# Kernel tuning notes

Hardware: AMD Instinct MI355X
Metric: run time of the kernel (lower is better)

## Reference

```python
import jax, jax.numpy as jnp
import numpy as np

NUM_CAT = 16
SEG_LENS = np.array([4, 2, 2, 4, 4, 3, 3, 2, 4, 6, 2, 6, 3, 3, 3, 3], dtype=np.int64)
SHIFTS = np.concatenate([[0], np.cumsum(SEG_LENS)[:-1]]).astype(np.int64)
MAX_SEG_COUNT = int(SEG_LENS.max())           # 6
MAX_SEG = int(SHIFTS[-1] + SEG_LENS[-1] - 1)  # 53
IN = 128
N = 65536
EPS = 1e-5  # BatchNorm1d default eps
SLOPE = 0.2  # LeakyReLU negative slope


def setup_inputs() -> dict:
    key = jax.random.key(0)
    ks = jax.random.split(key, 4)
    features = jax.random.normal(ks[0], (N, IN), dtype=jnp.float32)
    category_labels = jax.random.randint(ks[1], (N,), 0, NUM_CAT, dtype=jnp.int64)
    # channel raising MLP: Linear(IN -> NUM_CAT*IN, bias=False)
    W1 = jax.random.normal(ks[2], (IN, NUM_CAT * IN), dtype=jnp.float32) * (1.0 / np.sqrt(IN))
    gamma = jnp.ones((NUM_CAT * IN,), dtype=jnp.float32)
    beta = jnp.zeros((NUM_CAT * IN,), dtype=jnp.float32)
    # UnaryConv weight: xavier_normal over (NUM_CAT, IN, MAX_SEG_COUNT)
    W2 = jax.random.normal(ks[3], (NUM_CAT, IN, MAX_SEG_COUNT), dtype=jnp.float32) * np.sqrt(2.0 / (IN + MAX_SEG_COUNT))
    bias = jnp.zeros((MAX_SEG_COUNT,), dtype=jnp.float32)
    return dict(features=features, W1=W1, gamma=gamma, beta=beta, W2=W2, bias=bias,
                category_labels=category_labels)


def reference(features, W1, gamma, beta, W2, bias, category_labels):
    n = features.shape[0]
    # channel raising: Linear -> BatchNorm1d (batch stats) -> LeakyReLU(0.2)
    h = features @ W1                                   # [N, C*D]
    mean = h.mean(axis=0)
    var = h.var(axis=0)                                 # biased, as in torch BN
    h = (h - mean) / jnp.sqrt(var + EPS) * gamma + beta
    h = jnp.where(h >= 0, h, SLOPE * h)
    # per-category batched matmul classifier
    h = h.reshape(n, NUM_CAT, IN).transpose(1, 0, 2)    # [C, N, D]
    logits_all = jnp.einsum('cnd,cds->cns', h, W2) + bias  # [C, N, S]
    n_idx = jnp.arange(n)
    logits = logits_all[category_labels, n_idx]         # gather: [N, S]
    logsm = jax.nn.log_softmax(logits, axis=-1)
    # scatter into per-category segment ranges of the [N, MAX_SEG+1] output
    shifts = jnp.asarray(SHIFTS)[category_labels]       # [N]
    seg_len = jnp.asarray(SEG_LENS)[category_labels]    # [N]
    s_idx = jnp.arange(MAX_SEG_COUNT)
    valid = s_idx[None, :] < seg_len[:, None]           # [N, S]
    cols = jnp.clip(shifts[:, None] + s_idx[None, :], 0, MAX_SEG)
    vals = jnp.where(valid, logsm, 0.0)                 # invalid slots add 0
    out = jnp.zeros((n, MAX_SEG + 1), dtype=logsm.dtype)
    out = out.at[n_idx[:, None], cols].add(vals)
    return out
```

## Files before the change

### kernel.cpp

```cpp
#include <hip/hip_runtime.h>
#include <hip/hip_bf16.h>

#define NCAT 16

typedef __attribute__((ext_vector_type(8))) short short8v;
typedef __attribute__((ext_vector_type(4))) float float4v;
typedef __attribute__((ext_vector_type(16))) float f32x16;

__constant__ int c_shift[NCAT] = {0,4,6,8,12,16,19,22,24,28,34,36,42,45,48,51};
__constant__ int c_len[NCAT]   = {4,2,2,4,4,3,3,2,4,6,2,6,3,3,3,3};


static inline __device__ unsigned pk2(float lo, float hi) {
  float2 f2; f2.x = lo; f2.y = hi;
  __hip_bfloat162 h = __float22bfloat162_rn(f2);
  unsigned u; __builtin_memcpy(&u, &h, 4);
  return u;
}
static inline __device__ float bf2f(unsigned short v) {
  unsigned u = (unsigned)v << 16;
  float f; __builtin_memcpy(&f, &u, 4);
  return f;
}

template<bool PART>
__global__ __launch_bounds__(1024) void k_stats_m(
    const float* __restrict__ F, const float* __restrict__ W1,
    float* __restrict__ Gdst, unsigned* __restrict__ Gp16,
    float* __restrict__ sv, float* __restrict__ svpart,
    unsigned short* __restrict__ Wlb)
{
  const int tid = threadIdx.x;
  if (blockIdx.x >= 256) {
    const int cat = (int)blockIdx.x - 256;
    for (int e = tid; e < 2048; e += 1024) {
      const int fid = e >> 6, l = e & 63;
      const int ks = fid >> 3, ct = fid & 7;
      const int kb = 32 * ks + 8 * (l >> 4);
      const int c = cat * 128 + 16 * ct + (l & 15);
      uint4 pk;
      pk.x = pk2(W1[(size_t)(kb + 0) * 2048 + c], W1[(size_t)(kb + 1) * 2048 + c]);
      pk.y = pk2(W1[(size_t)(kb + 2) * 2048 + c], W1[(size_t)(kb + 3) * 2048 + c]);
      pk.z = pk2(W1[(size_t)(kb + 4) * 2048 + c], W1[(size_t)(kb + 5) * 2048 + c]);
      pk.w = pk2(W1[(size_t)(kb + 6) * 2048 + c], W1[(size_t)(kb + 7) * 2048 + c]);
      *(uint4*)(Wlb + ((size_t)(cat * 32 + fid) * 64 + l) * 8) = pk;
    }
    return;
  }

  const int rowbase = blockIdx.x * 256;
  const int wid = tid >> 6, lane = tid & 63;
  const int wi = wid >> 2, wj = wid & 3;
  const int i0 = wi * 32, j0 = wj * 32;
  const int lr = lane & 31, lh = lane >> 5;

  f32x16 acc;
  #pragma unroll
  for (int e = 0; e < 16; ++e) acc[e] = 0.f;
  float svacc = 0.f;

  for (int ch = 0; ch < 8; ++ch) {
    #pragma unroll
    for (int h = 0; h < 2; ++h) {
      const int rbase = rowbase + ch * 32 + 16 * h + 8 * lh;
      float fa[8], fb[8];
      #pragma unroll
      for (int j = 0; j < 8; ++j) {
        const float* rp = F + (size_t)(rbase + j) * 128;
        fa[j] = rp[i0 + lr];
        fb[j] = rp[j0 + lr];
      }
      if (wj == 0) {
        #pragma unroll
        for (int j = 0; j < 8; ++j) svacc += fa[j];
      }
      uint4 av4, bv4;
      av4.x = pk2(fa[0], fa[1]); av4.y = pk2(fa[2], fa[3]);
      av4.z = pk2(fa[4], fa[5]); av4.w = pk2(fa[6], fa[7]);
      bv4.x = pk2(fb[0], fb[1]); bv4.y = pk2(fb[2], fb[3]);
      bv4.z = pk2(fb[4], fb[5]); bv4.w = pk2(fb[6], fb[7]);
      acc = __builtin_amdgcn_mfma_f32_32x32x16_bf16(
          __builtin_bit_cast(short8v, av4), __builtin_bit_cast(short8v, bv4),
          acc, 0, 0, 0);
    }
  }

  if (wj == 0) {
    svacc += __shfl_xor(svacc, 32);
    if (lane < 32) {
      if (PART) svpart[blockIdx.x * 128 + i0 + lr] = svacc;
      else      atomicAdd(&sv[i0 + lr], svacc);
    }
  }

  if (PART) {
    unsigned* gp = Gp16 + (size_t)blockIdx.x * 8192;
    #pragma unroll
    for (int t = 0; t < 8; ++t) {
      const int rowe = ((2 * t) & 3) + 8 * (t >> 1) + 4 * lh;
      gp[((i0 + rowe) >> 1) * 128 + j0 + lr] = pk2(acc[2 * t], acc[2 * t + 1]);
    }
  } else {
    #pragma unroll
    for (int reg = 0; reg < 16; ++reg) {
      const int row = (reg & 3) + 8 * (reg >> 2) + 4 * lh;
      atomicAdd(&Gdst[(i0 + row) * 128 + j0 + lr], acc[reg]);
    }
  }
}

__global__ __launch_bounds__(256) void k_reduce(
    const unsigned* __restrict__ Gp16, const float* __restrict__ svpart,
    float* __restrict__ G, float* __restrict__ sv)
{
  const int b = blockIdx.x, tid = threadIdx.x;
  if (b < 64) {
    const int e = b * 128 + (tid >> 1);
    const int half = tid & 1;
    float lo = 0.f, hi = 0.f;
    #pragma unroll 4
    for (int p = half * 128; p < half * 128 + 128; ++p) {
      const unsigned u = Gp16[(size_t)p * 8192 + e];
      lo += bf2f((unsigned short)(u & 0xffffu));
      hi += bf2f((unsigned short)(u >> 16));
    }
    lo += __shfl_xor(lo, 1);
    hi += __shfl_xor(hi, 1);
    if (half == 0) {
      const int pr = e >> 7, col = e & 127;
      G[(2 * pr) * 128 + col]     = lo;
      G[(2 * pr + 1) * 128 + col] = hi;
    }
  } else {
    if (tid < 128) {
      float s = 0.f;
      #pragma unroll 8
      for (int p = 0; p < 256; ++p) s += svpart[p * 128 + tid];
      sv[tid] = s;
    }
  }
}

__global__ __launch_bounds__(256) void k_params(
    const float* __restrict__ G, const float* __restrict__ sv,
    const float* __restrict__ W1, const float* __restrict__ gamma,
    const float* __restrict__ beta, float* __restrict__ scale,
    float* __restrict__ shiftv)
{
  __shared__ float Gl[128][133];
  __shared__ float Wl[128][16];
  __shared__ float redq[16][16];
  __shared__ float redm[16][16];
  const int tid = threadIdx.x;
  const int jb = blockIdx.x * 16;
  for (int i = tid; i < 16384; i += 256) Gl[i >> 7][i & 127] = G[i];
  for (int i = tid; i < 2048; i += 256) {
    int k = i >> 4, col = i & 15;
    Wl[k][col] = W1[(size_t)k * 2048 + jb + col];
  }
  __syncthreads();
  const int col = tid & 15, part = tid >> 4;
  float msq = 0.f, mean = 0.f;
  for (int ii = 0; ii < 8; ++ii) {
    const int i = part * 8 + ii;
    const float wi = Wl[i][col];
    float inner = 0.f;
    #pragma unroll 8
    for (int k = 0; k < 128; ++k) inner = fmaf(Gl[i][k], Wl[k][col], inner);
    msq = fmaf(wi, inner, msq);
  }
  #pragma unroll
  for (int kk = 0; kk < 8; ++kk) {
    const int k = part * 8 + kk;
    mean = fmaf(sv[k], Wl[k][col], mean);
  }
  redq[part][col] = msq;
  redm[part][col] = mean;
  __syncthreads();
  if (tid < 16) {
    float q = 0.f, m = 0.f;
    #pragma unroll
    for (int p = 0; p < 16; ++p) { q += redq[p][tid]; m += redm[p][tid]; }
    m *= (1.f / 65536.f);
    q *= (1.f / 65536.f);
    float var = q - m * m;
    float sc = gamma[jb + tid] * rsqrtf(var + 1e-5f);
    scale[jb + tid] = sc;
    shiftv[jb + tid] = beta[jb + tid] - m * sc;
  }
}

__global__ __launch_bounds__(512, 4) void k_main(
    const float* __restrict__ F, const unsigned short* __restrict__ Wlb,
    const float* __restrict__ W2, const float* __restrict__ bias,
    const float* __restrict__ scale, const float* __restrict__ shiftv,
    const int* __restrict__ lab, float* __restrict__ out)
{
  __shared__ float W2l[16 * 784];
  __shared__ float obuf[128 * 54];
  __shared__ unsigned short lrows[128];
  __shared__ int wcs[2][NCAT];
  __shared__ int loff[NCAT + 1];
  __shared__ unsigned char gcat[32], gsub[32];
  __shared__ int gtot;

  const int tid = threadIdx.x;
  const int blk = (int)blockIdx.x;
  const int wid = tid >> 6, lane = tid & 63;
  const int lrow = lane & 15, lhi = lane >> 4;

  for (int i = tid; i < 12288; i += 512) {
    const int cat = i / 768;
    const int r = i - cat * 768;
    const int c = r / 6, s = r - c * 6;
    W2l[cat * 784 + c * 6 + s + (c >> 3)] = W2[i];
  }
  for (int i = tid; i < 6912; i += 512) obuf[i] = 0.f;

  int myc = 0, myrank = 0;
  if (tid < 128) {
    myc = lab[blk * 128 + tid];
    const unsigned long long lanebit = 1ull << lane;
    #pragma unroll
    for (int cc = 0; cc < NCAT; ++cc) {
      unsigned long long m = __ballot(myc == cc);
      if (lane == 0) wcs[wid][cc] = (int)__popcll(m);
      if (myc == cc) myrank = (int)__popcll(m & (lanebit - 1));
    }
  }
  __syncthreads();
  if (tid == 0) {
    int a = 0, g = 0;
    for (int c = 0; c < NCAT; ++c) {
      loff[c] = a;
      const int cnt = wcs[0][c] + wcs[1][c];
      for (int s2 = 0; s2 * 16 < cnt; ++s2) {
        gcat[g] = (unsigned char)c; gsub[g] = (unsigned char)s2; ++g;
      }
      a += cnt;
    }
    loff[NCAT] = a;
    gtot = g;
  }
  __syncthreads();
  if (tid < 128) {
    const int slot = loff[myc] + ((tid >= 64) ? wcs[0][myc] : 0) + myrank;
    lrows[slot] = (unsigned short)tid;
  }
  __syncthreads();

  float bi[6];
  #pragma unroll
  for (int s = 0; s < 6; ++s) bi[s] = bias[s];

  const int ng = gtot;
  for (int g = wid; g < ng; g += 8) {
    const int cat = gcat[g];
    const int slot0 = loff[cat] + ((int)gsub[g] << 4);
    const int hi2 = loff[cat + 1];
    const int navail = min(16, hi2 - slot0);
    const int srow = lrows[min(slot0 + lrow, hi2 - 1)];
    const float* fp = F + ((size_t)(blk * 128 + srow)) * 128 + lhi * 8;
    const unsigned short* wbase = Wlb + (size_t)cat * 16384;

    float4v acc[8];
    #pragma unroll
    for (int ct = 0; ct < 8; ++ct) acc[ct] = (float4v){0.f, 0.f, 0.f, 0.f};

    #pragma unroll
    for (int ks = 0; ks < 4; ++ks) {
      const float4 a0 = *(const float4*)(fp + ks * 32);
      const float4 a1 = *(const float4*)(fp + ks * 32 + 4);
      uint4 av4;
      av4.x = pk2(a0.x, a0.y); av4.y = pk2(a0.z, a0.w);
      av4.z = pk2(a1.x, a1.y); av4.w = pk2(a1.z, a1.w);
      const short8v av = __builtin_bit_cast(short8v, av4);
      #pragma unroll
      for (int ct = 0; ct < 8; ++ct) {
        short8v bv = *(const short8v*)(wbase + ((ks * 8 + ct) * 64 + lane) * 8);
        acc[ct] = __builtin_amdgcn_mfma_f32_16x16x32_bf16(av, bv, acc[ct], 0, 0, 0);
      }
    }

    float p[4][6];
    #pragma unroll
    for (int j = 0; j < 4; ++j)
      #pragma unroll
      for (int s = 0; s < 6; ++s) p[j][s] = 0.f;
    #pragma unroll
    for (int ct = 0; ct < 8; ++ct) {
      const int c = ct * 16 + lrow;
      const float s_ = scale[cat * 128 + c];
      const float h_ = shiftv[cat * 128 + c];
      float w2v[6];
      #pragma unroll
      for (int s = 0; s < 6; ++s) w2v[s] = W2l[cat * 784 + c * 6 + s + (c >> 3)];
      #pragma unroll
      for (int j = 0; j < 4; ++j) {
        float a = acc[ct][j] * s_ + h_;
        a = (a >= 0.f) ? a : 0.2f * a;
        #pragma unroll
        for (int s = 0; s < 6; ++s) p[j][s] = fmaf(a, w2v[s], p[j][s]);
      }
    }
    const bool b1 = (lrow & 1) != 0;
    const bool b2 = (lrow & 2) != 0;
    float q[2][6], r[6];
    #pragma unroll
    for (int t = 0; t < 2; ++t)
      #pragma unroll
      for (int s = 0; s < 6; ++s) {
        float snd = b1 ? p[2 * t][s] : p[2 * t + 1][s];
        float kp  = b1 ? p[2 * t + 1][s] : p[2 * t][s];
        q[t][s] = kp + __shfl_xor(snd, 1);
      }
    #pragma unroll
    for (int s = 0; s < 6; ++s) {
      float snd = b2 ? q[0][s] : q[1][s];
      float kp  = b2 ? q[1][s] : q[0][s];
      r[s] = kp + __shfl_xor(snd, 2);
    }
    #pragma unroll
    for (int s = 0; s < 6; ++s) r[s] += __shfl_xor(r[s], 4);
    #pragma unroll
    for (int s = 0; s < 6; ++s) r[s] += __shfl_xor(r[s], 8);

    const int jj = lrow & 3, sb = lrow >> 2;
    const int jrow = 4 * lhi + jj;
    float pj[6];
    #pragma unroll
    for (int s = 0; s < 6; ++s) pj[s] = r[s] + bi[s];
    float mx = fmaxf(fmaxf(fmaxf(pj[0], pj[1]), fmaxf(pj[2], pj[3])), fmaxf(pj[4], pj[5]));
    float e = __expf(pj[0] - mx) + __expf(pj[1] - mx) + __expf(pj[2] - mx)
            + __expf(pj[3] - mx) + __expf(pj[4] - mx) + __expf(pj[5] - mx);
    float lse = mx + __logf(e);

    if (jrow < navail) {
      const int orow = (int)lrows[slot0 + jrow];
      const int shc = c_shift[cat], lnc = c_len[cat];
      float* ob = obuf + orow * 54 + shc;
      if (sb == 0) {
        ob[0] = pj[0] - lse;
        ob[1] = pj[1] - lse;
        if (lnc > 2) ob[2] = pj[2] - lse;
        if (lnc > 3) ob[3] = pj[3] - lse;
      } else if (sb == 1) {
        if (lnc > 4) ob[4] = pj[4] - lse;
        if (lnc > 5) ob[5] = pj[5] - lse;
      }
    }
  }
  __syncthreads();

  const float2* ob2 = (const float2*)obuf;
  float2* o2 = (float2*)(out + (size_t)blk * 6912);
  for (int i = tid; i < 3456; i += 512) o2[i] = ob2[i];
}

extern "C" void kernel_launch(void* const* d_in, const int* in_sizes, int n_in,
                              void* d_out, int out_size, void* d_ws, size_t ws_size,
                              hipStream_t stream) {
  const float* F     = (const float*)d_in[0];
  const float* W1    = (const float*)d_in[1];
  const float* gamma = (const float*)d_in[2];
  const float* beta  = (const float*)d_in[3];
  const float* W2    = (const float*)d_in[4];
  const float* bias  = (const float*)d_in[5];
  const int*   lab   = (const int*)d_in[6];
  float* out = (float*)d_out;

  char* ws = (char*)d_ws;
  float* scale   = (float*)(ws + 0);
  float* shiftv  = (float*)(ws + 8192);
  float* G       = (float*)(ws + 16384);
  float* sv      = (float*)(ws + 81920);
  unsigned short* Wlb = (unsigned short*)(ws + 82432);
  unsigned* Gp16 = (unsigned*)(ws + 606720);
  float* svpart  = (float*)(ws + 8995328);

  const size_t need = 9126400;
  if (ws_size >= need) {
    hipLaunchKernelGGL(k_stats_m<true>, dim3(272), dim3(1024), 0, stream,
                       F, W1, G, Gp16, sv, svpart, Wlb);
    hipLaunchKernelGGL(k_reduce, dim3(65), dim3(256), 0, stream,
                       Gp16, svpart, G, sv);
  } else {
    hipMemsetAsync(ws + 16384, 0, 66048, stream);
    hipLaunchKernelGGL(k_stats_m<false>, dim3(272), dim3(1024), 0, stream,
                       F, W1, G, Gp16, sv, svpart, Wlb);
  }
  hipLaunchKernelGGL(k_params, dim3(128), dim3(256), 0, stream,
                     G, sv, W1, gamma, beta, scale, shiftv);
  hipLaunchKernelGGL(k_main, dim3(512), dim3(512), 0, stream,
                     F, Wlb, W2, bias, scale, shiftv, lab, out);
}
```

Before: 73.93 us.

## Prepack W2 in global memory and halve k_main block size to raise occupancy

The W2 classifier weights are now padded to 8 floats per channel by the prep blocks of the stats kernel and read by k_main directly from global/L2 with float4 loads. Previously each k_main block staged all of W2 into ~49KB of shared memory. k_main is also reshaped to 64 rows per block with 256 threads and 1024 blocks, which shrinks LDS use so more blocks fit per CU. The risk is extra global/L2 traffic for W2 reads in the epilogue. Smaller blocks also mean fewer rows per category, so MFMA tiles are more often partially filled, adding wasted work.

```diff
diff --git a/kernel.cpp b/kernel.cpp
--- a/kernel.cpp
+++ b/kernel.cpp
@@ -26,9 +26,10 @@
 template<bool PART>
 __global__ __launch_bounds__(1024) void k_stats_m(
     const float* __restrict__ F, const float* __restrict__ W1,
+    const float* __restrict__ W2,
     float* __restrict__ Gdst, unsigned* __restrict__ Gp16,
     float* __restrict__ sv, float* __restrict__ svpart,
-    unsigned short* __restrict__ Wlb)
+    unsigned short* __restrict__ Wlb, float* __restrict__ W2p)
 {
   const int tid = threadIdx.x;
   if (blockIdx.x >= 256) {
@@ -44,6 +45,10 @@
       pk.z = pk2(W1[(size_t)(kb + 4) * 2048 + c], W1[(size_t)(kb + 5) * 2048 + c]);
       pk.w = pk2(W1[(size_t)(kb + 6) * 2048 + c], W1[(size_t)(kb + 7) * 2048 + c]);
       *(uint4*)(Wlb + ((size_t)(cat * 32 + fid) * 64 + l) * 8) = pk;
+    }
+    if (tid < 1024) {
+      const int c = tid >> 3, s = tid & 7;
+      W2p[cat * 1024 + tid] = (s < 6) ? W2[cat * 768 + c * 6 + s] : 0.f;
     }
     return;
   }
@@ -190,16 +195,15 @@
   }
 }
 
-__global__ __launch_bounds__(512, 4) void k_main(
+__global__ __launch_bounds__(256, 4) void k_main(
     const float* __restrict__ F, const unsigned short* __restrict__ Wlb,
-    const float* __restrict__ W2, const float* __restrict__ bias,
+    const float* __restrict__ W2p, const float* __restrict__ bias,
     const float* __restrict__ scale, const float* __restrict__ shiftv,
     const int* __restrict__ lab, float* __restrict__ out)
 {
-  __shared__ float W2l[16 * 784];
-  __shared__ float obuf[128 * 54];
-  __shared__ unsigned short lrows[128];
-  __shared__ int wcs[2][NCAT];
+  __shared__ float obuf[64 * 54];
+  __shared__ unsigned short lrows[64];
+  __shared__ int wcs[NCAT];
   __shared__ int loff[NCAT + 1];
   __shared__ unsigned char gcat[32], gsub[32];
   __shared__ int gtot;
@@ -209,22 +213,19 @@
   const int wid = tid >> 6, lane = tid & 63;
   const int lrow = lane & 15, lhi = lane >> 4;
 
-  for (int i = tid; i < 12288; i += 512) {
-    const int cat = i / 768;
-    const int r = i - cat * 768;
-    const int c = r / 6, s = r - c * 6;
-    W2l[cat * 784 + c * 6 + s + (c >> 3)] = W2[i];
-  }
-  for (int i = tid; i < 6912; i += 512) obuf[i] = 0.f;
+  {
+    float2* ob2 = (float2*)obuf;
+    for (int i = tid; i < 1728; i += 256) ob2[i] = make_float2(0.f, 0.f);
+  }
 
   int myc = 0, myrank = 0;
-  if (tid < 128) {
-    myc = lab[blk * 128 + tid];
+  if (tid < 64) {
+    myc = lab[blk * 64 + tid];
     const unsigned long long lanebit = 1ull << lane;
     #pragma unroll
     for (int cc = 0; cc < NCAT; ++cc) {
       unsigned long long m = __ballot(myc == cc);
-      if (lane == 0) wcs[wid][cc] = (int)__popcll(m);
+      if (lane == 0) wcs[cc] = (int)__popcll(m);
       if (myc == cc) myrank = (int)__popcll(m & (lanebit - 1));
     }
   }
@@ -233,7 +234,7 @@
     int a = 0, g = 0;
     for (int c = 0; c < NCAT; ++c) {
       loff[c] = a;
-      const int cnt = wcs[0][c] + wcs[1][c];
+      const int cnt = wcs[c];
       for (int s2 = 0; s2 * 16 < cnt; ++s2) {
         gcat[g] = (unsigned char)c; gsub[g] = (unsigned char)s2; ++g;
       }
@@ -243,10 +244,7 @@
     gtot = g;
   }
   __syncthreads();
-  if (tid < 128) {
-    const int slot = loff[myc] + ((tid >= 64) ? wcs[0][myc] : 0) + myrank;
-    lrows[slot] = (unsigned short)tid;
-  }
+  if (tid < 64) lrows[loff[myc] + myrank] = (unsigned short)tid;
   __syncthreads();
 
   float bi[6];
@@ -254,13 +252,13 @@
   for (int s = 0; s < 6; ++s) bi[s] = bias[s];
 
   const int ng = gtot;
-  for (int g = wid; g < ng; g += 8) {
+  for (int g = wid; g < ng; g += 4) {
     const int cat = gcat[g];
     const int slot0 = loff[cat] + ((int)gsub[g] << 4);
     const int hi2 = loff[cat + 1];
     const int navail = min(16, hi2 - slot0);
     const int srow = lrows[min(slot0 + lrow, hi2 - 1)];
-    const float* fp = F + ((size_t)(blk * 128 + srow)) * 128 + lhi * 8;
+    const float* fp = F + ((size_t)(blk * 64 + srow)) * 128 + lhi * 8;
     const unsigned short* wbase = Wlb + (size_t)cat * 16384;
 
     float4v acc[8];
@@ -292,9 +290,10 @@
       const int c = ct * 16 + lrow;
       const float s_ = scale[cat * 128 + c];
       const float h_ = shiftv[cat * 128 + c];
-      float w2v[6];
-      #pragma unroll
-      for (int s = 0; s < 6; ++s) w2v[s] = W2l[cat * 784 + c * 6 + s + (c >> 3)];
+      const float4* w2p4 = (const float4*)(W2p + ((size_t)cat * 128 + c) * 8);
+      const float4 wa = w2p4[0];
+      const float4 wb = w2p4[1];
+      const float w2v[6] = {wa.x, wa.y, wa.z, wa.w, wb.x, wb.y};
       #pragma unroll
       for (int j = 0; j < 4; ++j) {
         float a = acc[ct][j] * s_ + h_;
@@ -353,8 +352,8 @@
   __syncthreads();
 
   const float2* ob2 = (const float2*)obuf;
-  float2* o2 = (float2*)(out + (size_t)blk * 6912);
-  for (int i = tid; i < 3456; i += 512) o2[i] = ob2[i];
+  float2* o2 = (float2*)(out + (size_t)blk * 3456);
+  for (int i = tid; i < 1728; i += 256) o2[i] = ob2[i];
 }
 
 extern "C" void kernel_launch(void* const* d_in, const int* in_sizes, int n_in,
@@ -375,22 +374,23 @@
   float* G       = (float*)(ws + 16384);
   float* sv      = (float*)(ws + 81920);
   unsigned short* Wlb = (unsigned short*)(ws + 82432);
-  unsigned* Gp16 = (unsigned*)(ws + 606720);
-  float* svpart  = (float*)(ws + 8995328);
-
-  const size_t need = 9126400;
+  float* W2p     = (float*)(ws + 606720);
+  unsigned* Gp16 = (unsigned*)(ws + 672256);
+  float* svpart  = (float*)(ws + 9060864);
+
+  const size_t need = 9191936;
   if (ws_size >= need) {
     hipLaunchKernelGGL(k_stats_m<true>, dim3(272), dim3(1024), 0, stream,
-                       F, W1, G, Gp16, sv, svpart, Wlb);
+                       F, W1, W2, G, Gp16, sv, svpart, Wlb, W2p);
     hipLaunchKernelGGL(k_reduce, dim3(65), dim3(256), 0, stream,
                        Gp16, svpart, G, sv);
   } else {
     hipMemsetAsync(ws + 16384, 0, 66048, stream);
     hipLaunchKernelGGL(k_stats_m<false>, dim3(272), dim3(1024), 0, stream,
-                       F, W1, G, Gp16, sv, svpart, Wlb);
+                       F, W1, W2, G, Gp16, sv, svpart, Wlb, W2p);
   }
   hipLaunchKernelGGL(k_params, dim3(128), dim3(256), 0, stream,
                      G, sv, W1, gamma, beta, scale, shiftv);
-  hipLaunchKernelGGL(k_main, dim3(512), dim3(512), 0, stream,
-                     F, Wlb, W2, bias, scale, shiftv, lab, out);
-}
+  hipLaunchKernelGGL(k_main, dim3(1024), dim3(256), 0, stream,
+                     F, Wlb, W2p, bias, scale, shiftv, lab, out);
+}
```

Result: slower. 89.42 us (+21.0%).
